# Kernel optimization log

Measured on AMD Instinct MI355X. Metric: run time of the kernel, lower is better.

Reference implementation:

```python
import jax, jax.numpy as jnp
import numpy as np

KEY_DIM = 512
VALUE_DIM = 128
CAPACITY = 500000
N_RETRIEVE = 32
LN_EPS = 1e-5       # torch nn.LayerNorm default
NORM_EPS = 1e-12    # torch F.normalize default


def setup_inputs() -> dict:
    key = jax.random.key(0)
    ks = jax.random.split(key, 5)
    w_scale = 0.02
    return {
        "query": jax.random.normal(ks[0], (1, KEY_DIM), dtype=jnp.float32),
        "W1": jax.random.normal(ks[1], (KEY_DIM, KEY_DIM), dtype=jnp.float32) * w_scale,
        "b1": jnp.zeros((KEY_DIM,), dtype=jnp.float32),
        "W2": jax.random.normal(ks[2], (KEY_DIM, KEY_DIM), dtype=jnp.float32) * w_scale,
        "b2": jnp.zeros((KEY_DIM,), dtype=jnp.float32),
        "ln_g": jnp.ones((KEY_DIM,), dtype=jnp.float32),
        "ln_b": jnp.zeros((KEY_DIM,), dtype=jnp.float32),
        "keys": jax.random.normal(ks[3], (CAPACITY, KEY_DIM), dtype=jnp.float32),
        "values": jax.random.normal(ks[4], (CAPACITY, VALUE_DIM), dtype=jnp.float32),
    }


def _l2_normalize(x, axis=-1):
    # matches torch F.normalize: x / max(||x||, eps)
    n = jnp.linalg.norm(x, axis=axis, keepdims=True)
    return x / jnp.maximum(n, NORM_EPS)


def _layer_norm(x, g, b):
    mu = jnp.mean(x, axis=-1, keepdims=True)
    var = jnp.mean(jnp.square(x - mu), axis=-1, keepdims=True)
    return (x - mu) * jax.lax.rsqrt(var + LN_EPS) * g + b


def reference(query, W1, b1, W2, b2, ln_g, ln_b, keys, values):
    # EpisodicMemory.read_aggregated with a full memory bank (n == capacity).
    q_in = jax.lax.stop_gradient(query)                 # query.detach()
    h = jax.nn.silu(q_in @ W1.T + b1) @ W2.T + b2       # key_proj MLP, [1, K]
    h = _layer_norm(h, ln_g, ln_b)                      # key_norm
    q = _l2_normalize(h)[0]                             # [K]
    kn = _l2_normalize(keys)                            # [C, K]
    sim = kn @ q                                        # cosine sims, [C]
    top_sim, top_idx = jax.lax.top_k(sim, N_RETRIEVE)   # [k], [k]
    vals = values[top_idx]                              # gather, [k, V]
    attn = jax.nn.softmax(top_sim, axis=0)              # [k]
    return jnp.sum(vals * attn[:, None], axis=0)        # [V]
```

## Files before the change

### kernel.cpp

```cpp
#include <hip/hip_runtime.h>
#include <math.h>

#define KEY_DIM   512
#define VALUE_DIM 128
#define CAPACITY  500000
#define NRET      32
#define LN_EPS    1e-5f
#define NORM_EPS  1e-12f
#define NEG_INF   (-3.402823466e38f)
#define IDX_INF   0x7fffffff

#define SCAN_BLOCKS 2048
#define CHUNK       245
#define JMAX        62


template<int CTRL>
__device__ inline float dppMovF(float x) {
  return __int_as_float(__builtin_amdgcn_update_dpp(0, __float_as_int(x), CTRL, 0xF, 0xF, true));
}

__device__ inline float waveSumF(float x) {
  x += dppMovF<0xB1>(x);
  x += dppMovF<0x4E>(x);
  x += dppMovF<0x124>(x);
  x += dppMovF<0x128>(x);
  x += __int_as_float(__builtin_amdgcn_ds_swizzle(__float_as_int(x), 0x401F));
  x += __shfl_xor(x, 32);
  return x;
}

template<int D>
__device__ inline int fetchI(int x) {
  if constexpr (D == 1)       return __builtin_amdgcn_update_dpp(0, x, 0xB1, 0xF, 0xF, true);
  else if constexpr (D == 2)  return __builtin_amdgcn_update_dpp(0, x, 0x4E, 0xF, 0xF, true);
  else if constexpr (D == 4)  return __builtin_amdgcn_ds_swizzle(x, 0x101F);
  else if constexpr (D == 8)  return __builtin_amdgcn_ds_swizzle(x, 0x201F);
  else if constexpr (D == 16) return __builtin_amdgcn_ds_swizzle(x, 0x401F);
  else                        return __shfl_xor(x, 32);
}
template<int D>
__device__ inline float fetchF(float x) { return __int_as_float(fetchI<D>(__float_as_int(x))); }

__device__ inline void waveArgMax3(float& v, int& gi, int& code) {
  #pragma unroll
  for (int off = 32; off; off >>= 1) {
    float ov = __shfl_xor(v, off);
    int   og = __shfl_xor(gi, off);
    int   oc = __shfl_xor(code, off);
    if (ov > v || (ov == v && og < gi)) { v = ov; gi = og; code = oc; }
  }
}

__device__ inline float blockSum512(float v, float* red) {
  #pragma unroll
  for (int off = 32; off; off >>= 1) v += __shfl_xor(v, off);
  int wid = threadIdx.x >> 6, lane = threadIdx.x & 63;
  if (lane == 0) red[wid] = v;
  __syncthreads();
  float s = red[0] + red[1] + red[2] + red[3] + red[4] + red[5] + red[6] + red[7];
  __syncthreads();
  return s;
}


__global__ __launch_bounds__(256) void matvec1_kernel(
    const float* __restrict__ query, const float* __restrict__ W1,
    const float* __restrict__ b1, float* __restrict__ h)
{
  int tid = threadIdx.x, wid = tid >> 6, lane = tid & 63;
  int row = (blockIdx.x << 2) + wid;
  const float4* q4 = (const float4*)query;
  const float4* wrow = (const float4*)(W1 + (size_t)row * KEY_DIM);
  float4 a0 = wrow[lane],      q0 = q4[lane];
  float4 a1 = wrow[lane + 64], q1 = q4[lane + 64];
  float acc = a0.x*q0.x + a0.y*q0.y + a0.z*q0.z + a0.w*q0.w
            + a1.x*q1.x + a1.y*q1.y + a1.z*q1.z + a1.w*q1.w;
  #pragma unroll
  for (int off = 32; off; off >>= 1) acc += __shfl_xor(acc, off);
  if (lane == 0) {
    float x = acc + b1[row];
    h[row] = x / (1.f + expf(-x));
  }
}

__global__ __launch_bounds__(256) void matvec2_kernel(
    const float* __restrict__ h, const float* __restrict__ W2,
    const float* __restrict__ b2, float* __restrict__ g)
{
  int tid = threadIdx.x, wid = tid >> 6, lane = tid & 63;
  int row = (blockIdx.x << 2) + wid;
  const float4* h4 = (const float4*)h;
  const float4* wrow = (const float4*)(W2 + (size_t)row * KEY_DIM);
  float4 a0 = wrow[lane],      q0 = h4[lane];
  float4 a1 = wrow[lane + 64], q1 = h4[lane + 64];
  float acc = a0.x*q0.x + a0.y*q0.y + a0.z*q0.z + a0.w*q0.w
            + a1.x*q1.x + a1.y*q1.y + a1.z*q1.z + a1.w*q1.w;
  #pragma unroll
  for (int off = 32; off; off >>= 1) acc += __shfl_xor(acc, off);
  if (lane == 0) g[row] = acc + b2[row];
}

__global__ __launch_bounds__(512) void norm_kernel(
    const float* __restrict__ g, const float* __restrict__ ln_g,
    const float* __restrict__ ln_b, float* __restrict__ qn)
{
  __shared__ float red[8];
  int tid = threadIdx.x;
  float x  = g[tid];
  float mu = blockSum512(x, red) * (1.f / 512.f);
  float d  = x - mu;
  float var = blockSum512(d * d, red) * (1.f / 512.f);
  float y  = d * (1.f / sqrtf(var + LN_EPS)) * ln_g[tid] + ln_b[tid];
  float nsq = blockSum512(y * y, red);
  float n  = fmaxf(sqrtf(nsq), NORM_EPS);
  qn[tid] = y / n;
}


__global__ __launch_bounds__(256) void scan_topk(
    const float* __restrict__ keys, const float* __restrict__ qn,
    float* __restrict__ cand_val, int* __restrict__ cand_idx, int C)
{
  int tid = threadIdx.x, wid = tid >> 6, lane = tid & 63;
  int s0  = blockIdx.x * CHUNK;

  const float4* q4 = (const float4*)qn;
  float4 q0 = q4[lane];
  float4 q1 = q4[lane + 64];
  const float4* keys4 = (const float4*)keys;

  float v  = NEG_INF;
  int   gi = IDX_INF;

  #pragma unroll 2
  for (int j = 0; j < JMAX; ++j) {
    int row   = s0 + wid + (j << 2);
    bool valid = row < C;
    int rc    = valid ? row : (C - 1);
    const float4* kr = keys4 + (size_t)rc * 128;
    float4 a = kr[lane];
    float4 c = kr[lane + 64];
    float dot = a.x*q0.x + a.y*q0.y + a.z*q0.z + a.w*q0.w
              + c.x*q1.x + c.y*q1.y + c.z*q1.z + c.w*q1.w;
    float ss  = a.x*a.x + a.y*a.y + a.z*a.z + a.w*a.w
              + c.x*c.x + c.y*c.y + c.z*c.z + c.w*c.w;
    dot = waveSumF(dot);
    ss  = waveSumF(ss);
    float sim = dot / fmaxf(sqrtf(ss), NORM_EPS);
    if (lane == j) {
      v  = valid ? sim : NEG_INF;
      gi = valid ? row : IDX_INF;
    }
  }

  #define BSTAGE(D, K) { \
    float ov = fetchF<D>(v); int og = fetchI<D>(gi); \
    bool keepL = ((lane & (D)) == 0) == ((lane & (K)) == 0); \
    bool ogt = (ov > v) || (ov == v && og < gi); \
    bool take = keepL ? ogt : !ogt; \
    if (take) { v = ov; gi = og; } }

  BSTAGE(1,2)
  BSTAGE(2,4)  BSTAGE(1,4)
  BSTAGE(4,8)  BSTAGE(2,8)  BSTAGE(1,8)
  BSTAGE(8,16) BSTAGE(4,16) BSTAGE(2,16) BSTAGE(1,16)
  BSTAGE(16,32) BSTAGE(8,32) BSTAGE(4,32) BSTAGE(2,32) BSTAGE(1,32)
  BSTAGE(32,64) BSTAGE(16,64) BSTAGE(8,64) BSTAGE(4,64) BSTAGE(2,64) BSTAGE(1,64)
  #undef BSTAGE

  if (lane < NRET) {
    int w = (blockIdx.x << 2) + wid;
    cand_val[w * NRET + lane] = v;
    cand_idx[w * NRET + lane] = gi;
  }
}


__global__ __launch_bounds__(256) void merge_topk(
    const float* __restrict__ in_val, const int* __restrict__ in_idx,
    float* __restrict__ out_val, int* __restrict__ out_idx)
{
  __shared__ float cv[1024];
  __shared__ int   ci[1024];
  __shared__ float redv[4];
  __shared__ int   redg[4];
  __shared__ int   redp[4];
  int tid = threadIdx.x, wid = tid >> 6, lane = tid & 63;
  int base = blockIdx.x << 10;
  for (int t = tid; t < 1024; t += 256) { cv[t] = in_val[base + t]; ci[t] = in_idx[base + t]; }
  __syncthreads();

  for (int it = 0; it < NRET; ++it) {
    float bv = NEG_INF; int bg = IDX_INF; int bp = -1;
    #pragma unroll
    for (int k = 0; k < 4; ++k) {
      int p = tid + (k << 8);
      float vv = cv[p]; int gg = ci[p];
      if (vv > bv || (vv == bv && gg < bg)) { bv = vv; bg = gg; bp = p; }
    }
    waveArgMax3(bv, bg, bp);
    if (lane == 0) { redv[wid] = bv; redg[wid] = bg; redp[wid] = bp; }
    __syncthreads();
    if (tid == 0) {
      float vv = redv[0]; int gg = redg[0]; int pp = redp[0];
      #pragma unroll
      for (int i = 1; i < 4; ++i)
        if (redv[i] > vv || (redv[i] == vv && redg[i] < gg)) { vv = redv[i]; gg = redg[i]; pp = redp[i]; }
      out_val[(blockIdx.x << 5) + it] = vv;
      out_idx[(blockIdx.x << 5) + it] = gg;
      if (pp >= 0) cv[pp] = NEG_INF;
    }
    __syncthreads();
  }
}


__global__ __launch_bounds__(256) void final_kernel(
    const float* __restrict__ c3v, const int* __restrict__ c3i,
    const float* __restrict__ values, float* __restrict__ out)
{
  __shared__ float selv[NRET];
  __shared__ int   seli[NRET];
  __shared__ float attn[NRET];
  int tid = threadIdx.x, wid = tid >> 6, lane = tid & 63;

  if (wid == 0) {
    float v0 = c3v[lane], v1 = c3v[lane + 64], v2 = c3v[lane + 128], v3 = c3v[lane + 192];
    int   g0 = c3i[lane], g1 = c3i[lane + 64], g2 = c3i[lane + 128], g3 = c3i[lane + 192];
    for (int it = 0; it < NRET; ++it) {
      float bv = v0; int bg = g0; int bc = 0;
      if (v1 > bv || (v1 == bv && g1 < bg)) { bv = v1; bg = g1; bc = 1; }
      if (v2 > bv || (v2 == bv && g2 < bg)) { bv = v2; bg = g2; bc = 2; }
      if (v3 > bv || (v3 == bv && g3 < bg)) { bv = v3; bg = g3; bc = 3; }
      int code = (lane << 2) | bc;
      waveArgMax3(bv, bg, code);
      if (lane == (code >> 2)) {
        int s = code & 3;
        if (s == 0) v0 = NEG_INF; else if (s == 1) v1 = NEG_INF;
        else if (s == 2) v2 = NEG_INF; else v3 = NEG_INF;
      }
      if (lane == 0) { selv[it] = bv; seli[it] = bg; }
    }
  }
  __syncthreads();

  if (tid < NRET) {
    float e = expf(selv[tid] - selv[0]);
    float s = e;
    #pragma unroll
    for (int off = 16; off; off >>= 1) s += __shfl_xor(s, off);
    attn[tid] = e / s;
  }
  __syncthreads();

  if (tid < VALUE_DIM) {
    float acc = 0.f;
    #pragma unroll
    for (int k = 0; k < NRET; ++k)
      acc += attn[k] * values[(size_t)seli[k] * VALUE_DIM + tid];
    out[tid] = acc;
  }
}


extern "C" void kernel_launch(void* const* d_in, const int* in_sizes, int n_in,
                              void* d_out, int out_size, void* d_ws, size_t ws_size,
                              hipStream_t stream) {
  const float* query  = (const float*)d_in[0];
  const float* W1     = (const float*)d_in[1];
  const float* b1     = (const float*)d_in[2];
  const float* W2     = (const float*)d_in[3];
  const float* b2     = (const float*)d_in[4];
  const float* ln_g   = (const float*)d_in[5];
  const float* ln_b   = (const float*)d_in[6];
  const float* keys   = (const float*)d_in[7];
  const float* values = (const float*)d_in[8];
  float* out = (float*)d_out;

  float* wsf = (float*)d_ws;
  float* qn       = wsf;
  float* h        = wsf + 512;
  float* g        = wsf + 1024;
  float* cand_val = wsf + 2048;
  int*   cand_idx = (int*)(wsf + 2048 + 262144);
  float* c2v      = wsf + 2048 + 524288;
  int*   c2i      = (int*)(wsf + 2048 + 524288 + 8192);
  float* c3v      = wsf + 2048 + 524288 + 16384;
  int*   c3i      = (int*)(wsf + 2048 + 524288 + 16384 + 256);

  hipLaunchKernelGGL(matvec1_kernel, dim3(128), dim3(256), 0, stream, query, W1, b1, h);
  hipLaunchKernelGGL(matvec2_kernel, dim3(128), dim3(256), 0, stream, h, W2, b2, g);
  hipLaunchKernelGGL(norm_kernel,    dim3(1),   dim3(512), 0, stream, g, ln_g, ln_b, qn);
  hipLaunchKernelGGL(scan_topk,      dim3(SCAN_BLOCKS), dim3(256), 0, stream,
                     keys, qn, cand_val, cand_idx, CAPACITY);
  hipLaunchKernelGGL(merge_topk,     dim3(256), dim3(256), 0, stream,
                     cand_val, cand_idx, c2v, c2i);
  hipLaunchKernelGGL(merge_topk,     dim3(8),   dim3(256), 0, stream,
                     c2v, c2i, c3v, c3i);
  hipLaunchKernelGGL(final_kernel,   dim3(1),   dim3(256), 0, stream,
                     c3v, c3i, values, out);
}
```

Measured before the change: 299.3 us.

## Fuse layernorm into scan, batch key loads, and restructure top-k merge tree

Folds the LayerNorm and L2 normalisation into every scan block (each wave recomputes them), removing the separate norm kernel. The scan now gives each wave 256 rows, loaded 8 rows at a time for more memory-level parallelism, and uses a 256-element bitonic sort across four registers. This cuts the candidate count and allows a single wave-parallel merge stage plus a final kernel instead of two serial shared-memory merges. It trades redundant per-block norm work and higher register pressure for fewer launches and less merge traffic.

```diff
diff --git a/kernel.cpp b/kernel.cpp
--- a/kernel.cpp
+++ b/kernel.cpp
@@ -3,16 +3,17 @@
 
 #define KEY_DIM   512
 #define VALUE_DIM 128
-#define CAPACITY  500000
+#define CAP       500000
 #define NRET      32
 #define LN_EPS    1e-5f
 #define NORM_EPS  1e-12f
 #define NEG_INF   (-3.402823466e38f)
 #define IDX_INF   0x7fffffff
 
-#define SCAN_BLOCKS 2048
-#define CHUNK       245
-#define JMAX        62
+#define SCAN_BLOCKS 489
+#define NCAND       (SCAN_BLOCKS * 4 * 32)
+#define M1_BLOCKS   62
+#define N2          (M1_BLOCKS * 32)
 
 
 template<int CTRL>
@@ -42,25 +43,30 @@
 template<int D>
 __device__ inline float fetchF(float x) { return __int_as_float(fetchI<D>(__float_as_int(x))); }
 
-__device__ inline void waveArgMax3(float& v, int& gi, int& code) {
-  #pragma unroll
-  for (int off = 32; off; off >>= 1) {
-    float ov = __shfl_xor(v, off);
-    int   og = __shfl_xor(gi, off);
-    int   oc = __shfl_xor(code, off);
-    if (ov > v || (ov == v && og < gi)) { v = ov; gi = og; code = oc; }
-  }
-}
-
-__device__ inline float blockSum512(float v, float* red) {
-  #pragma unroll
-  for (int off = 32; off; off >>= 1) v += __shfl_xor(v, off);
-  int wid = threadIdx.x >> 6, lane = threadIdx.x & 63;
-  if (lane == 0) red[wid] = v;
-  __syncthreads();
-  float s = red[0] + red[1] + red[2] + red[3] + red[4] + red[5] + red[6] + red[7];
-  __syncthreads();
-  return s;
+template<int D>
+__device__ inline void amStep(float& v, int& g, int& c) {
+  float ov = fetchF<D>(v); int og = fetchI<D>(g); int oc = fetchI<D>(c);
+  if (ov > v || (ov == v && og < g)) { v = ov; g = og; c = oc; }
+}
+__device__ inline void waveArgMax3(float& v, int& g, int& c) {
+  amStep<1>(v, g, c); amStep<2>(v, g, c); amStep<4>(v, g, c);
+  amStep<8>(v, g, c); amStep<16>(v, g, c); amStep<32>(v, g, c);
+}
+
+template<int D>
+__device__ inline void ceStageLane(float& v, int& gi, bool desc, int lane) {
+  float ov = fetchF<D>(v); int og = fetchI<D>(gi);
+  bool better  = (ov > v) || (ov == v && og < gi);
+  bool amLower = (lane & D) == 0;
+  bool keepMax = (amLower == desc);
+  if (keepMax == better) { v = ov; gi = og; }
+}
+
+__device__ inline void ceStageReg(float& vA, int& gA, float& vB, int& gB, bool desc) {
+  bool better = (vB > vA) || (vB == vA && gB < gA);
+  bool sw = (better == desc);
+  float tv = sw ? vB : vA; vB = sw ? vA : vB; vA = tv;
+  int   tg = sw ? gB : gA; gB = sw ? gA : gB; gA = tg;
 }
 
 
@@ -76,8 +82,7 @@
   float4 a1 = wrow[lane + 64], q1 = q4[lane + 64];
   float acc = a0.x*q0.x + a0.y*q0.y + a0.z*q0.z + a0.w*q0.w
             + a1.x*q1.x + a1.y*q1.y + a1.z*q1.z + a1.w*q1.w;
-  #pragma unroll
-  for (int off = 32; off; off >>= 1) acc += __shfl_xor(acc, off);
+  acc = waveSumF(acc);
   if (lane == 0) {
     float x = acc + b1[row];
     h[row] = x / (1.f + expf(-x));
@@ -96,155 +101,227 @@
   float4 a1 = wrow[lane + 64], q1 = h4[lane + 64];
   float acc = a0.x*q0.x + a0.y*q0.y + a0.z*q0.z + a0.w*q0.w
             + a1.x*q1.x + a1.y*q1.y + a1.z*q1.z + a1.w*q1.w;
+  acc = waveSumF(acc);
+  if (lane == 0) g[row] = acc + b2[row];
+}
+
+
+__global__ __launch_bounds__(256, 4) void scan_kernel(
+    const float* __restrict__ keys, const float* __restrict__ g,
+    const float* __restrict__ ln_g, const float* __restrict__ ln_b,
+    float* __restrict__ cand_val, int* __restrict__ cand_idx)
+{
+  const int tid = threadIdx.x, wid = tid >> 6, lane = tid & 63;
+
+  const float4* g4 = (const float4*)g;
+  float4 x0 = g4[lane], x1 = g4[lane + 64];
+  float psum = x0.x + x0.y + x0.z + x0.w + x1.x + x1.y + x1.z + x1.w;
+  float mu = waveSumF(psum) * (1.f / 512.f);
+  float4 d0, d1;
+  d0.x = x0.x - mu; d0.y = x0.y - mu; d0.z = x0.z - mu; d0.w = x0.w - mu;
+  d1.x = x1.x - mu; d1.y = x1.y - mu; d1.z = x1.z - mu; d1.w = x1.w - mu;
+  float pvar = d0.x*d0.x + d0.y*d0.y + d0.z*d0.z + d0.w*d0.w
+             + d1.x*d1.x + d1.y*d1.y + d1.z*d1.z + d1.w*d1.w;
+  float var  = waveSumF(pvar) * (1.f / 512.f);
+  float rstd = 1.f / sqrtf(var + LN_EPS);
+  const float4* lg4 = (const float4*)ln_g;
+  const float4* lb4 = (const float4*)ln_b;
+  float4 a0 = lg4[lane], a1 = lg4[lane + 64];
+  float4 b0 = lb4[lane], b1 = lb4[lane + 64];
+  float4 y0, y1;
+  y0.x = d0.x*rstd*a0.x + b0.x; y0.y = d0.y*rstd*a0.y + b0.y;
+  y0.z = d0.z*rstd*a0.z + b0.z; y0.w = d0.w*rstd*a0.w + b0.w;
+  y1.x = d1.x*rstd*a1.x + b1.x; y1.y = d1.y*rstd*a1.y + b1.y;
+  y1.z = d1.z*rstd*a1.z + b1.z; y1.w = d1.w*rstd*a1.w + b1.w;
+  float pn  = y0.x*y0.x + y0.y*y0.y + y0.z*y0.z + y0.w*y0.w
+            + y1.x*y1.x + y1.y*y1.y + y1.z*y1.z + y1.w*y1.w;
+  float nsq = waveSumF(pn);
+  float nf  = 1.f / fmaxf(sqrtf(nsq), NORM_EPS);
+  float4 q0, q1;
+  q0.x = y0.x*nf; q0.y = y0.y*nf; q0.z = y0.z*nf; q0.w = y0.w*nf;
+  q1.x = y1.x*nf; q1.y = y1.y*nf; q1.z = y1.z*nf; q1.w = y1.w*nf;
+
+  const char* kl = (const char*)keys + (size_t)lane * 16;
+  const int wrow0 = (blockIdx.x << 10) + (wid << 8);
+
+  float sv[4]; int sg[4];
+
   #pragma unroll
-  for (int off = 32; off; off >>= 1) acc += __shfl_xor(acc, off);
-  if (lane == 0) g[row] = acc + b2[row];
-}
-
-__global__ __launch_bounds__(512) void norm_kernel(
-    const float* __restrict__ g, const float* __restrict__ ln_g,
-    const float* __restrict__ ln_b, float* __restrict__ qn)
-{
-  __shared__ float red[8];
-  int tid = threadIdx.x;
-  float x  = g[tid];
-  float mu = blockSum512(x, red) * (1.f / 512.f);
-  float d  = x - mu;
-  float var = blockSum512(d * d, red) * (1.f / 512.f);
-  float y  = d * (1.f / sqrtf(var + LN_EPS)) * ln_g[tid] + ln_b[tid];
-  float nsq = blockSum512(y * y, red);
-  float n  = fmaxf(sqrtf(nsq), NORM_EPS);
-  qn[tid] = y / n;
-}
-
-
-__global__ __launch_bounds__(256) void scan_topk(
-    const float* __restrict__ keys, const float* __restrict__ qn,
-    float* __restrict__ cand_val, int* __restrict__ cand_idx, int C)
-{
-  int tid = threadIdx.x, wid = tid >> 6, lane = tid & 63;
-  int s0  = blockIdx.x * CHUNK;
-
-  const float4* q4 = (const float4*)qn;
-  float4 q0 = q4[lane];
-  float4 q1 = q4[lane + 64];
-  const float4* keys4 = (const float4*)keys;
-
-  float v  = NEG_INF;
-  int   gi = IDX_INF;
-
-  #pragma unroll 2
-  for (int j = 0; j < JMAX; ++j) {
-    int row   = s0 + wid + (j << 2);
-    bool valid = row < C;
-    int rc    = valid ? row : (C - 1);
-    const float4* kr = keys4 + (size_t)rc * 128;
-    float4 a = kr[lane];
-    float4 c = kr[lane + 64];
-    float dot = a.x*q0.x + a.y*q0.y + a.z*q0.z + a.w*q0.w
-              + c.x*q1.x + c.y*q1.y + c.z*q1.z + c.w*q1.w;
-    float ss  = a.x*a.x + a.y*a.y + a.z*a.z + a.w*a.w
-              + c.x*c.x + c.y*c.y + c.z*c.z + c.w*c.w;
-    dot = waveSumF(dot);
-    ss  = waveSumF(ss);
-    float sim = dot / fmaxf(sqrtf(ss), NORM_EPS);
-    if (lane == j) {
-      v  = valid ? sim : NEG_INF;
-      gi = valid ? row : IDX_INF;
-    }
-  }
-
-  #define BSTAGE(D, K) { \
-    float ov = fetchF<D>(v); int og = fetchI<D>(gi); \
-    bool keepL = ((lane & (D)) == 0) == ((lane & (K)) == 0); \
-    bool ogt = (ov > v) || (ov == v && og < gi); \
-    bool take = keepL ? ogt : !ogt; \
-    if (take) { v = ov; gi = og; } }
-
-  BSTAGE(1,2)
-  BSTAGE(2,4)  BSTAGE(1,4)
-  BSTAGE(4,8)  BSTAGE(2,8)  BSTAGE(1,8)
-  BSTAGE(8,16) BSTAGE(4,16) BSTAGE(2,16) BSTAGE(1,16)
-  BSTAGE(16,32) BSTAGE(8,32) BSTAGE(4,32) BSTAGE(2,32) BSTAGE(1,32)
-  BSTAGE(32,64) BSTAGE(16,64) BSTAGE(8,64) BSTAGE(4,64) BSTAGE(2,64) BSTAGE(1,64)
-  #undef BSTAGE
+  for (int seg = 0; seg < 4; ++seg) {
+    const int segbase = wrow0 + (seg << 6);
+    float simreg = NEG_INF;
+    #pragma unroll 1
+    for (int bi = 0; bi < 8; ++bi) {
+      const int r0 = segbase + (bi << 3);
+      float4 A[8], B[8];
+      #pragma unroll
+      for (int i = 0; i < 8; ++i) {
+        int rr = min(r0 + i, CAP - 1);
+        const char* rp = kl + (size_t)rr * 2048;
+        A[i] = *(const float4*)rp;
+        B[i] = *(const float4*)(rp + 1024);
+      }
+      float dt[8], sq[8];
+      #pragma unroll
+      for (int i = 0; i < 8; ++i) {
+        dt[i] = A[i].x*q0.x + A[i].y*q0.y + A[i].z*q0.z + A[i].w*q0.w
+              + B[i].x*q1.x + B[i].y*q1.y + B[i].z*q1.z + B[i].w*q1.w;
+        sq[i] = A[i].x*A[i].x + A[i].y*A[i].y + A[i].z*A[i].z + A[i].w*A[i].w
+              + B[i].x*B[i].x + B[i].y*B[i].y + B[i].z*B[i].z + B[i].w*B[i].w;
+      }
+      #pragma unroll
+      for (int i = 0; i < 8; ++i) { dt[i] = waveSumF(dt[i]); sq[i] = waveSumF(sq[i]); }
+      #pragma unroll
+      for (int i = 0; i < 8; ++i) {
+        float sim = dt[i] / fmaxf(sqrtf(sq[i]), NORM_EPS);
+        bool ok = (r0 + i) < CAP;
+        sim = ok ? sim : NEG_INF;
+        int rb = (bi << 3) + i;
+        simreg = (lane == rb) ? sim : simreg;
+      }
+    }
+    sv[seg] = simreg;
+    sg[seg] = segbase + lane;
+  }
+
+  #define LST4(D, A0, A1, A2, A3) \
+    ceStageLane<D>(sv[0], sg[0], A0, lane); \
+    ceStageLane<D>(sv[1], sg[1], A1, lane); \
+    ceStageLane<D>(sv[2], sg[2], A2, lane); \
+    ceStageLane<D>(sv[3], sg[3], A3, lane);
+
+  { bool dm = (lane & 2) == 0;  LST4(1, dm,dm,dm,dm) }
+  { bool dm = (lane & 4) == 0;  LST4(2, dm,dm,dm,dm)  LST4(1, dm,dm,dm,dm) }
+  { bool dm = (lane & 8) == 0;  LST4(4, dm,dm,dm,dm)  LST4(2, dm,dm,dm,dm)
+                                LST4(1, dm,dm,dm,dm) }
+  { bool dm = (lane & 16) == 0; LST4(8, dm,dm,dm,dm)  LST4(4, dm,dm,dm,dm)
+                                LST4(2, dm,dm,dm,dm)  LST4(1, dm,dm,dm,dm) }
+  { bool dm = (lane & 32) == 0; LST4(16, dm,dm,dm,dm) LST4(8, dm,dm,dm,dm)
+                                LST4(4, dm,dm,dm,dm)  LST4(2, dm,dm,dm,dm)
+                                LST4(1, dm,dm,dm,dm) }
+  LST4(32, true,false,true,false) LST4(16, true,false,true,false)
+  LST4(8,  true,false,true,false) LST4(4,  true,false,true,false)
+  LST4(2,  true,false,true,false) LST4(1,  true,false,true,false)
+  ceStageReg(sv[0], sg[0], sv[1], sg[1], true);
+  ceStageReg(sv[2], sg[2], sv[3], sg[3], false);
+  LST4(32, true,true,false,false) LST4(16, true,true,false,false)
+  LST4(8,  true,true,false,false) LST4(4,  true,true,false,false)
+  LST4(2,  true,true,false,false) LST4(1,  true,true,false,false)
+  ceStageReg(sv[0], sg[0], sv[2], sg[2], true);
+  ceStageReg(sv[1], sg[1], sv[3], sg[3], true);
+  ceStageReg(sv[0], sg[0], sv[1], sg[1], true);
+  ceStageReg(sv[2], sg[2], sv[3], sg[3], true);
+  LST4(32, true,true,true,true) LST4(16, true,true,true,true)
+  LST4(8,  true,true,true,true) LST4(4,  true,true,true,true)
+  LST4(2,  true,true,true,true) LST4(1,  true,true,true,true)
+  #undef LST4
 
   if (lane < NRET) {
     int w = (blockIdx.x << 2) + wid;
-    cand_val[w * NRET + lane] = v;
-    cand_idx[w * NRET + lane] = gi;
-  }
-}
-
-
-__global__ __launch_bounds__(256) void merge_topk(
-    const float* __restrict__ in_val, const int* __restrict__ in_idx,
+    cand_val[w * NRET + lane] = sv[0];
+    cand_idx[w * NRET + lane] = sg[0];
+  }
+}
+
+
+__global__ __launch_bounds__(256) void merge_kernel(
+    const float* __restrict__ in_val, const int* __restrict__ in_idx, int n,
     float* __restrict__ out_val, int* __restrict__ out_idx)
 {
-  __shared__ float cv[1024];
-  __shared__ int   ci[1024];
-  __shared__ float redv[4];
-  __shared__ int   redg[4];
-  __shared__ int   redp[4];
+  __shared__ float lv[128];
+  __shared__ int   li[128];
   int tid = threadIdx.x, wid = tid >> 6, lane = tid & 63;
-  int base = blockIdx.x << 10;
-  for (int t = tid; t < 1024; t += 256) { cv[t] = in_val[base + t]; ci[t] = in_idx[base + t]; }
+
+  float vs[4]; int gs[4];
+  int base = (blockIdx.x << 10) + (wid << 8);
+  #pragma unroll
+  for (int k = 0; k < 4; ++k) {
+    int idx = base + (k << 6) + lane;
+    bool ok = idx < n;
+    vs[k] = ok ? in_val[idx] : NEG_INF;
+    gs[k] = ok ? in_idx[idx] : IDX_INF;
+  }
+  for (int it = 0; it < NRET; ++it) {
+    float bv = vs[0]; int bg = gs[0]; int bs = 0;
+    #pragma unroll
+    for (int k = 1; k < 4; ++k)
+      if (vs[k] > bv || (vs[k] == bv && gs[k] < bg)) { bv = vs[k]; bg = gs[k]; bs = k; }
+    int code = (lane << 2) | bs;
+    waveArgMax3(bv, bg, code);
+    if (lane == (code >> 2)) {
+      int s = code & 3;
+      if (s == 0) vs[0] = NEG_INF; else if (s == 1) vs[1] = NEG_INF;
+      else if (s == 2) vs[2] = NEG_INF; else vs[3] = NEG_INF;
+    }
+    if (lane == 0) { lv[(wid << 5) + it] = bv; li[(wid << 5) + it] = bg; }
+  }
   __syncthreads();
-
-  for (int it = 0; it < NRET; ++it) {
-    float bv = NEG_INF; int bg = IDX_INF; int bp = -1;
-    #pragma unroll
-    for (int k = 0; k < 4; ++k) {
-      int p = tid + (k << 8);
-      float vv = cv[p]; int gg = ci[p];
-      if (vv > bv || (vv == bv && gg < bg)) { bv = vv; bg = gg; bp = p; }
-    }
-    waveArgMax3(bv, bg, bp);
-    if (lane == 0) { redv[wid] = bv; redg[wid] = bg; redp[wid] = bp; }
-    __syncthreads();
-    if (tid == 0) {
-      float vv = redv[0]; int gg = redg[0]; int pp = redp[0];
-      #pragma unroll
-      for (int i = 1; i < 4; ++i)
-        if (redv[i] > vv || (redv[i] == vv && redg[i] < gg)) { vv = redv[i]; gg = redg[i]; pp = redp[i]; }
-      out_val[(blockIdx.x << 5) + it] = vv;
-      out_idx[(blockIdx.x << 5) + it] = gg;
-      if (pp >= 0) cv[pp] = NEG_INF;
-    }
-    __syncthreads();
+  if (wid == 0) {
+    float c0 = lv[lane], c1 = lv[64 + lane];
+    int   h0 = li[lane], h1 = li[64 + lane];
+    for (int it = 0; it < NRET; ++it) {
+      bool p1 = (c1 > c0) || (c1 == c0 && h1 < h0);
+      float bv = p1 ? c1 : c0; int bg = p1 ? h1 : h0;
+      int code = (lane << 1) | (p1 ? 1 : 0);
+      waveArgMax3(bv, bg, code);
+      if (lane == (code >> 1)) { if (code & 1) c1 = NEG_INF; else c0 = NEG_INF; }
+      if (lane == 0) {
+        out_val[(blockIdx.x << 5) + it] = bv;
+        out_idx[(blockIdx.x << 5) + it] = bg;
+      }
+    }
   }
 }
 
 
 __global__ __launch_bounds__(256) void final_kernel(
-    const float* __restrict__ c3v, const int* __restrict__ c3i,
+    const float* __restrict__ c2v, const int* __restrict__ c2i, int n,
     const float* __restrict__ values, float* __restrict__ out)
 {
+  __shared__ float lv[128];
+  __shared__ int   li[128];
   __shared__ float selv[NRET];
   __shared__ int   seli[NRET];
   __shared__ float attn[NRET];
   int tid = threadIdx.x, wid = tid >> 6, lane = tid & 63;
 
+  float vs[8]; int gs[8];
+  int base = (wid << 9);
+  #pragma unroll
+  for (int k = 0; k < 8; ++k) {
+    int idx = base + (k << 6) + lane;
+    bool ok = idx < n;
+    vs[k] = ok ? c2v[idx] : NEG_INF;
+    gs[k] = ok ? c2i[idx] : IDX_INF;
+  }
+  for (int it = 0; it < NRET; ++it) {
+    float bv = vs[0]; int bg = gs[0]; int bs = 0;
+    #pragma unroll
+    for (int k = 1; k < 8; ++k)
+      if (vs[k] > bv || (vs[k] == bv && gs[k] < bg)) { bv = vs[k]; bg = gs[k]; bs = k; }
+    int code = (lane << 3) | bs;
+    waveArgMax3(bv, bg, code);
+    if (lane == (code >> 3)) {
+      int s = code & 7;
+      #pragma unroll
+      for (int k = 0; k < 8; ++k) if (k == s) vs[k] = NEG_INF;
+    }
+    if (lane == 0) { lv[(wid << 5) + it] = bv; li[(wid << 5) + it] = bg; }
+  }
+  __syncthreads();
   if (wid == 0) {
-    float v0 = c3v[lane], v1 = c3v[lane + 64], v2 = c3v[lane + 128], v3 = c3v[lane + 192];
-    int   g0 = c3i[lane], g1 = c3i[lane + 64], g2 = c3i[lane + 128], g3 = c3i[lane + 192];
+    float c0 = lv[lane], c1 = lv[64 + lane];
+    int   h0 = li[lane], h1 = li[64 + lane];
     for (int it = 0; it < NRET; ++it) {
-      float bv = v0; int bg = g0; int bc = 0;
-      if (v1 > bv || (v1 == bv && g1 < bg)) { bv = v1; bg = g1; bc = 1; }
-      if (v2 > bv || (v2 == bv && g2 < bg)) { bv = v2; bg = g2; bc = 2; }
-      if (v3 > bv || (v3 == bv && g3 < bg)) { bv = v3; bg = g3; bc = 3; }
-      int code = (lane << 2) | bc;
+      bool p1 = (c1 > c0) || (c1 == c0 && h1 < h0);
+      float bv = p1 ? c1 : c0; int bg = p1 ? h1 : h0;
+      int code = (lane << 1) | (p1 ? 1 : 0);
       waveArgMax3(bv, bg, code);
-      if (lane == (code >> 2)) {
-        int s = code & 3;
-        if (s == 0) v0 = NEG_INF; else if (s == 1) v1 = NEG_INF;
-        else if (s == 2) v2 = NEG_INF; else v3 = NEG_INF;
-      }
+      if (lane == (code >> 1)) { if (code & 1) c1 = NEG_INF; else c0 = NEG_INF; }
       if (lane == 0) { selv[it] = bv; seli[it] = bg; }
     }
   }
   __syncthreads();
-
   if (tid < NRET) {
     float e = expf(selv[tid] - selv[0]);
     float s = e;
@@ -253,7 +330,6 @@
     attn[tid] = e / s;
   }
   __syncthreads();
-
   if (tid < VALUE_DIM) {
     float acc = 0.f;
     #pragma unroll
@@ -279,25 +355,19 @@
   float* out = (float*)d_out;
 
   float* wsf = (float*)d_ws;
-  float* qn       = wsf;
-  float* h        = wsf + 512;
-  float* g        = wsf + 1024;
-  float* cand_val = wsf + 2048;
-  int*   cand_idx = (int*)(wsf + 2048 + 262144);
-  float* c2v      = wsf + 2048 + 524288;
-  int*   c2i      = (int*)(wsf + 2048 + 524288 + 8192);
-  float* c3v      = wsf + 2048 + 524288 + 16384;
-  int*   c3i      = (int*)(wsf + 2048 + 524288 + 16384 + 256);
+  float* h        = wsf;
+  float* g        = wsf + 512;
+  float* cand_val = wsf + 1024;
+  int*   cand_idx = (int*)(wsf + 1024 + NCAND);
+  float* c2v      = wsf + 1024 + 2 * NCAND;
+  int*   c2i      = (int*)(wsf + 1024 + 2 * NCAND + N2);
 
   hipLaunchKernelGGL(matvec1_kernel, dim3(128), dim3(256), 0, stream, query, W1, b1, h);
   hipLaunchKernelGGL(matvec2_kernel, dim3(128), dim3(256), 0, stream, h, W2, b2, g);
-  hipLaunchKernelGGL(norm_kernel,    dim3(1),   dim3(512), 0, stream, g, ln_g, ln_b, qn);
-  hipLaunchKernelGGL(scan_topk,      dim3(SCAN_BLOCKS), dim3(256), 0, stream,
-                     keys, qn, cand_val, cand_idx, CAPACITY);
-  hipLaunchKernelGGL(merge_topk,     dim3(256), dim3(256), 0, stream,
-                     cand_val, cand_idx, c2v, c2i);
-  hipLaunchKernelGGL(merge_topk,     dim3(8),   dim3(256), 0, stream,
-                     c2v, c2i, c3v, c3i);
-  hipLaunchKernelGGL(final_kernel,   dim3(1),   dim3(256), 0, stream,
-                     c3v, c3i, values, out);
-}
+  hipLaunchKernelGGL(scan_kernel, dim3(SCAN_BLOCKS), dim3(256), 0, stream,
+                     keys, g, ln_g, ln_b, cand_val, cand_idx);
+  hipLaunchKernelGGL(merge_kernel, dim3(M1_BLOCKS), dim3(256), 0, stream,
+                     cand_val, cand_idx, NCAND, c2v, c2i);
+  hipLaunchKernelGGL(final_kernel, dim3(1), dim3(256), 0, stream,
+                     c2v, c2i, N2, values, out);
+}
```

Measured after the change: 278.8 us, median of 2. 6.9% less time.
